# Optimization experiments

Measured on AMD Instinct MI355X. Metric: run time of the kernel, lower is better.

Reference implementation:

```python
import jax, jax.numpy as jnp
import numpy as np
import math

N, E, D, H = 1536, 49152, 512, 8
DH = D // H  # head dim = 64
SCALE = 256.0 * math.sqrt(2.0)  # rel_dists scaling in forward


def sinusoidal_pe(x, d):
    """x: [...] float positions -> [..., d] interleaved sin/cos encoding."""
    div = jnp.exp(jnp.arange(0, d, 2, dtype=jnp.float32) * (-math.log(10000.0) / d))
    ang = x[..., None] * div  # [..., d//2]
    return jnp.stack([jnp.sin(ang), jnp.cos(ang)], axis=-1).reshape(*x.shape, d)


def setup_inputs() -> dict:
    key = jax.random.key(0)
    ks = jax.random.split(key, 8)
    features = jax.random.normal(ks[0], (N, D), dtype=jnp.float32)
    edge_index = jax.random.randint(ks[1], (2, E), 0, N, dtype=jnp.int64)
    edge_attr = jax.random.uniform(ks[2], (E,), dtype=jnp.float32)  # normalized distances
    pos = jax.random.uniform(ks[3], (N, 2), dtype=jnp.float32)  # unused by forward
    s = 1.0 / math.sqrt(D)  # ~xavier-uniform bound sqrt(6/(D+D))... use simple symmetric init
    Wq = jax.random.uniform(ks[4], (D, D), minval=-s, maxval=s, dtype=jnp.float32)
    Wk = jax.random.uniform(ks[5], (D, D), minval=-s, maxval=s, dtype=jnp.float32)
    Wv = jax.random.uniform(ks[6], (D, D), minval=-s, maxval=s, dtype=jnp.float32)
    bq = jnp.zeros((D,), jnp.float32)
    bk = jnp.zeros((D,), jnp.float32)
    bv = jnp.zeros((D,), jnp.float32)
    return dict(features=features, edge_index=edge_index, edge_attr=edge_attr, pos=pos,
                Wq=Wq, bq=bq, Wk=Wk, bk=bk, Wv=Wv, bv=bv)


def reference(features, edge_index, edge_attr, pos, Wq, bq, Wk, bk, Wv, bv):
    # batch dim is 1 in the original (features.unsqueeze(0)); we omit it.
    q = (features @ Wq.T + bq).reshape(N, H, DH).transpose(1, 0, 2)  # [H,N,DH]
    k = (features @ Wk.T + bk).reshape(N, H, DH).transpose(1, 0, 2)
    v = (features @ Wv.T + bv).reshape(N, H, DH).transpose(1, 0, 2)

    qk = jnp.einsum('hqd,hrd->hqr', q, k)  # [H,N,N]

    # to_dense_adj: scatter-add edge_attr into dense [N,N], then scale
    rel = jnp.zeros((N, N), jnp.float32).at[edge_index[0], edge_index[1]].add(edge_attr) * SCALE
    # embed_k and embed_q are identical parameter-free sinusoidal encodings of rel
    rk = sinusoidal_pe(rel, DH)  # [N,N,DH]

    # original: qk + q.rk + k.rq + (q_repeat*k_repeat == qk)  => 2*qk + q.rk + k.rk
    logits = 2.0 * qk \
        + jnp.einsum('hqd,qrd->hqr', q, rk) \
        + jnp.einsum('hrd,qrd->hqr', k, rk)
    attn = jax.nn.softmax(logits / math.sqrt(DH), axis=-1)  # [H,N,N]

    out = jnp.einsum('hqr,hrd->hqd', attn, v)  # [H,N,DH]
    out = out.transpose(1, 0, 2).reshape(N, D)  # [N,D]
    return out.max(axis=0)  # [D] max-pool over nodes (MIL pooling)
```

## Files before the change

kernel.cpp:

```cpp
#include <hip/hip_runtime.h>
#include <cmath>


constexpr int Nn  = 1536;
constexpr int Dd  = 512;
constexpr int Hh  = 8;
constexpr int DHd = 64;
constexpr int SPLITS = 8;
constexpr float SCALE_F = 362.03867196751236f;
constexpr float M0 = 8.0f;
constexpr unsigned short NOEDGE = 0xFFFFu;

typedef float f4 __attribute__((ext_vector_type(4)));
typedef int   i4 __attribute__((ext_vector_type(4)));
typedef int   i2 __attribute__((ext_vector_type(2)));
typedef __attribute__((ext_vector_type(4))) float f32x4;
typedef __attribute__((ext_vector_type(8))) short bf16x8;

__device__ inline unsigned short bf16_rne(float x) {
    unsigned u = __float_as_uint(x);
    unsigned r = u + 0x7fff + ((u >> 16) & 1);
    return (unsigned short)(r >> 16);
}
__device__ inline float bf16_tof(unsigned short h) {
    return __uint_as_float(((unsigned)h) << 16);
}

__global__ __launch_bounds__(256) void pack_fw_k(
    const float* __restrict__ feat,
    const float* __restrict__ Wq, const float* __restrict__ Wk, const float* __restrict__ Wv,
    unsigned short* __restrict__ pFh, unsigned short* __restrict__ pFl,
    unsigned short* __restrict__ pWh, unsigned short* __restrict__ pWl)
{
    int tg = blockIdx.x * 256 + threadIdx.x;
    int type = blockIdx.y;
    int L = tg & 63;
    int kc = (tg >> 6) & 15;
    int t10 = tg >> 10;
    const float* src;
    unsigned short *oh, *ol;
    int row, col;
    if (type == 0) {
        src = feat; oh = pFh; ol = pFl;
        row = t10 * 16 + (L & 15);
        col = kc * 32 + (L >> 4) * 8;
    } else {
        int z = t10 >> 5, nt = t10 & 31;
        src = (z == 0) ? Wq : (z == 1) ? Wk : Wv;
        oh = pWh; ol = pWl;
        row = nt * 16 + (L & 15);
        col = kc * 32 + (L >> 4) * 8;
    }
    f4 a = *(const f4*)(src + (size_t)row * Dd + col);
    f4 b = *(const f4*)(src + (size_t)row * Dd + col + 4);
    float x[8];
    #pragma unroll
    for (int j = 0; j < 4; ++j) { x[j] = a[j]; x[4 + j] = b[j]; }
    unsigned short hs[8], ls[8];
    #pragma unroll
    for (int j = 0; j < 8; ++j) {
        hs[j] = bf16_rne(x[j]);
        ls[j] = bf16_rne(x[j] - bf16_tof(hs[j]));
    }
    *(bf16x8*)(oh + (size_t)tg * 8) = *(bf16x8*)hs;
    *(bf16x8*)(ol + (size_t)tg * 8) = *(bf16x8*)ls;
}

__global__ __launch_bounds__(256) void qkvm_k(
    const unsigned short* __restrict__ pFh, const unsigned short* __restrict__ pFl,
    const unsigned short* __restrict__ pWh, const unsigned short* __restrict__ pWl,
    const float* __restrict__ bq, const float* __restrict__ bk, const float* __restrict__ bv,
    float* __restrict__ Qo, float* __restrict__ Ko, float* __restrict__ Vo)
{
    const int lin = blockIdx.x + 8 * (blockIdx.y + 24 * blockIdx.z);
    const int swz = (lin & 7) * 72 + (lin >> 3);
    const int bx  = swz & 7;
    const int rem = swz >> 3;
    const int by  = rem % 24;
    const int bz  = rem / 24;

    const float* __restrict__ bias = (bz == 0) ? bq : (bz == 1) ? bk : bv;
    float* __restrict__ outp       = (bz == 0) ? Qo : (bz == 1) ? Ko : Vo;
    const int tid = threadIdx.x;
    const int L = tid & 63, wv = tid >> 6;
    const int l15 = L & 15, quad = L >> 4;
    const int mt0 = by * 4 + (wv & 1) * 2;
    const int nt0 = bx * 4 + (wv >> 1) * 2;

    f32x4 acc[2][2];
    #pragma unroll
    for (int i = 0; i < 2; ++i)
        #pragma unroll
        for (int j = 0; j < 2; ++j) acc[i][j] = (f32x4){0.f, 0.f, 0.f, 0.f};

    for (int kc = 0; kc < 16; ++kc) {
        bf16x8 ah[2], al[2], bh[2], bl[2];
        #pragma unroll
        for (int i = 0; i < 2; ++i) {
            size_t ao = ((size_t)((mt0 + i) * 16 + kc)) * 512 + L * 8;
            ah[i] = *(const bf16x8*)(pFh + ao);
            al[i] = *(const bf16x8*)(pFl + ao);
            size_t bo = ((size_t)((bz * 32 + nt0 + i) * 16 + kc)) * 512 + L * 8;
            bh[i] = *(const bf16x8*)(pWh + bo);
            bl[i] = *(const bf16x8*)(pWl + bo);
        }
        #pragma unroll
        for (int i = 0; i < 2; ++i)
            #pragma unroll
            for (int j = 0; j < 2; ++j) {
                f32x4 a = acc[i][j];
                a = __builtin_amdgcn_mfma_f32_16x16x32_bf16(ah[i], bh[j], a, 0, 0, 0);
                a = __builtin_amdgcn_mfma_f32_16x16x32_bf16(ah[i], bl[j], a, 0, 0, 0);
                a = __builtin_amdgcn_mfma_f32_16x16x32_bf16(al[i], bh[j], a, 0, 0, 0);
                a = __builtin_amdgcn_mfma_f32_16x16x32_bf16(al[i], bl[j], a, 0, 0, 0);
                acc[i][j] = a;
            }
    }

    #pragma unroll
    for (int i = 0; i < 2; ++i) {
        int row0 = (mt0 + i) * 16 + quad * 4;
        #pragma unroll
        for (int j = 0; j < 2; ++j) {
            int col = (nt0 + j) * 16 + l15;
            float b = bias[col];
            #pragma unroll
            for (int reg = 0; reg < 4; ++reg)
                outp[(size_t)(row0 + reg) * Dd + col] = acc[i][j][reg] + b;
        }
    }
}

__global__ __launch_bounds__(256) void pack_k(
    const float* __restrict__ Q, const float* __restrict__ K, const float* __restrict__ V,
    unsigned short* __restrict__ pQh, unsigned short* __restrict__ pQl,
    unsigned short* __restrict__ pKh, unsigned short* __restrict__ pKl,
    unsigned short* __restrict__ pVh, unsigned short* __restrict__ pVl)
{
    int tg = blockIdx.x * 256 + threadIdx.x;
    int type = blockIdx.y;
    int L = tg & 63;
    float x[8];
    unsigned short* oh;
    unsigned short* ol;
    if (type < 2) {
        const float* src = type ? K : Q;
        oh = type ? pKh : pQh;
        ol = type ? pKl : pQl;
        int kc = (tg >> 6) & 1;
        int mt = (tg >> 7) % 96;
        int h  = (tg >> 7) / 96;
        int row = mt * 16 + (L & 15);
        int col = h * 64 + kc * 32 + (L >> 4) * 8;
        f4 a = *(const f4*)(src + (size_t)row * Dd + col);
        f4 b = *(const f4*)(src + (size_t)row * Dd + col + 4);
        float sc = type ? 1.0f : 0.25f;
        #pragma unroll
        for (int j = 0; j < 4; ++j) { x[j] = a[j] * sc; x[4 + j] = b[j] * sc; }
    } else {
        oh = pVh; ol = pVl;
        int dt = (tg >> 6) & 3;
        int rc = (tg >> 8) % 48;
        int h  = (tg >> 8) / 48;
        int col  = h * 64 + dt * 16 + (L & 15);
        int row0 = rc * 32 + (L >> 4) * 8;
        #pragma unroll
        for (int j = 0; j < 8; ++j) x[j] = V[(size_t)(row0 + j) * Dd + col];
    }
    unsigned short hs[8], ls[8];
    #pragma unroll
    for (int j = 0; j < 8; ++j) {
        hs[j] = bf16_rne(x[j]);
        ls[j] = bf16_rne(x[j] - bf16_tof(hs[j]));
    }
    *(bf16x8*)(oh + (size_t)tg * 8) = *(bf16x8*)hs;
    *(bf16x8*)(ol + (size_t)tg * 8) = *(bf16x8*)ls;
}

__global__ __launch_bounds__(256) void init_rel_k(float* __restrict__ rel,
                                                  unsigned short* __restrict__ eid)
{
    size_t i = ((size_t)blockIdx.x * 256 + threadIdx.x) * 4;
    if (i < (size_t)Nn * Nn) {
        *(f4*)(rel + i) = (f4){0.f, 0.f, 0.f, 0.f};
        *(i2*)(eid + i) = (i2){-1, -1};
    }
}

__global__ __launch_bounds__(256) void scatter_k(
    const int* __restrict__ raw, const float* __restrict__ attr,
    float* __restrict__ rel, unsigned short* __restrict__ eid,
    int* __restrict__ idxn, int E)
{
    int e = blockIdx.x * 256 + threadIdx.x;
    if (e >= E) return;
    int acc = 0;
    #pragma unroll
    for (int i = 0; i < 16; ++i) acc |= raw[2 * i + 1];
    int s, t;
    if (acc == 0) { s = raw[2 * e]; t = raw[2 * (E + e)]; }
    else          { s = raw[e];     t = raw[E + e]; }
    idxn[e] = s; idxn[E + e] = t;
    size_t off = (size_t)s * Nn + t;
    atomicAdd(rel + off, attr[e] * SCALE_F);
    eid[off] = (unsigned short)e;
}

__global__ void oddsum_k(const float* __restrict__ Q, const float* __restrict__ K,
                         float* __restrict__ qodd, float* __restrict__ kodd,
                         float* __restrict__ koddT)
{
    int t = blockIdx.x * 256 + threadIdx.x;
    if (t >= 2 * Nn * Hh) return;
    const float* src = (t < Nn * Hh) ? Q : K;
    int i = (t < Nn * Hh) ? t : t - Nn * Hh;
    int n = i >> 3, h = i & 7;
    const float* row = src + (size_t)n * Dd + h * DHd;
    float s = 0.f;
    #pragma unroll
    for (int ii = 0; ii < 32; ++ii) s += row[2 * ii + 1];
    if (t < Nn * Hh) qodd[i] = s;
    else { kodd[i] = s; koddT[h * Nn + n] = 0.125f * s; }
}

__global__ __launch_bounds__(256) void delta2_k(
    const int* __restrict__ idxn, const float* __restrict__ rel,
    const float* __restrict__ Q, const float* __restrict__ K,
    const float* __restrict__ qodd, const float* __restrict__ kodd,
    float* __restrict__ delta8, int E)
{
    const int w = threadIdx.x >> 6;
    const int e = blockIdx.x * 4 + w;
    if (e >= E) return;
    const int j = threadIdx.x & 63;
    const int qi = idxn[e], ri = idxn[E + e];
    const float x = rel[(size_t)qi * Nn + ri];
    const float dj = __expf(-0.28782313662425572f * (float)(j >> 1));
    float sj, cj;
    __sincosf(x * dj, &sj, &cj);
    const float tj = (j & 1) ? cj : sj;
    const float* qrow = Q + (size_t)qi * Dd;
    const float* krow = K + (size_t)ri * Dd;
    float out = 0.f;
    #pragma unroll
    for (int h = 0; h < 8; ++h) {
        float v = (qrow[h * 64 + j] + krow[h * 64 + j]) * tj;
        #pragma unroll
        for (int o = 1; o < 64; o <<= 1) v += __shfl_xor(v, o);
        if (j == h) out = v;
    }
    if (j < 8)
        delta8[(size_t)e * Hh + j] = 0.125f * (out - qodd[qi * Hh + j] - kodd[ri * Hh + j]);
}

__global__ __launch_bounds__(256, 2) void flash6_k(
    const unsigned short* __restrict__ pQh, const unsigned short* __restrict__ pQl,
    const unsigned short* __restrict__ pKh, const unsigned short* __restrict__ pKl,
    const unsigned short* __restrict__ pVh, const unsigned short* __restrict__ pVl,
    const unsigned short* __restrict__ eid, const float* __restrict__ delta8,
    const float* __restrict__ koddT,
    float* __restrict__ Opart, float* __restrict__ Lpart)
{
    const int lin = blockIdx.x + 24 * (blockIdx.y + 8 * blockIdx.z);
    const int swz = (lin & 7) * 192 + (lin >> 3);
    const int qtb = swz % 24;
    const int hs  = swz / 24;
    const int h   = hs & 7;
    const int s   = hs >> 3;

    const int w   = threadIdx.x >> 6;
    const int qt  = qtb * 4 + w;
    const int L   = threadIdx.x & 63, quad = L >> 4, l15 = L & 15;
    const int q0  = qt * 16;
    __shared__ unsigned short phi[4][16][80];
    __shared__ unsigned short plo[4][16][80];

    bf16x8 qh[2], ql[2];
    #pragma unroll
    for (int kc = 0; kc < 2; ++kc) {
        size_t off = ((size_t)((h * 96 + qt) * 2 + kc)) * 512 + L * 8;
        qh[kc] = *(const bf16x8*)(pQh + off);
        ql[kc] = *(const bf16x8*)(pQl + off);
    }

    f32x4 O[4];
    float lsum[4];
    #pragma unroll
    for (int r = 0; r < 4; ++r) { lsum[r] = 0.f; O[r] = (f32x4){0.f, 0.f, 0.f, 0.f}; }

    const int NT = 24 / SPLITS;
    const int Tbase = s * NT;

    bf16x8 kh0[4], kh1[4], kl0[4], kl1[4];
    {
        const int r0 = Tbase * 64;
        #pragma unroll
        for (int nt = 0; nt < 4; ++nt) {
            size_t b0 = ((size_t)((h * 96 + (r0 >> 4) + nt) * 2)) * 512 + L * 8;
            kh0[nt] = *(const bf16x8*)(pKh + b0);
            kh1[nt] = *(const bf16x8*)(pKh + b0 + 512);
            kl0[nt] = *(const bf16x8*)(pKl + b0);
            kl1[nt] = *(const bf16x8*)(pKl + b0 + 512);
        }
    }

    float kvcur[4], dcur[16];
    {
        const int r0 = Tbase * 64;
        unsigned ecur[16];
        #pragma unroll
        for (int nt = 0; nt < 4; ++nt) {
            kvcur[nt] = koddT[h * Nn + r0 + nt * 16 + l15];
            #pragma unroll
            for (int reg = 0; reg < 4; ++reg)
                ecur[nt * 4 + reg] = eid[(size_t)(q0 + quad * 4 + reg) * Nn + r0 + nt * 16 + l15];
        }
        #pragma unroll
        for (int i = 0; i < 16; ++i) {
            unsigned e = ecur[i];
            float d = 0.f;
            if (e != NOEDGE) d = delta8[(size_t)e * Hh + h];
            dcur[i] = d;
        }
    }

    for (int T = 0; T < NT; ++T) {
        const int r0 = (Tbase + T) * 64;
        const bool more = (T + 1 < NT);

        unsigned enxt[16];
        float kvnxt[4];
        if (more) {
            const int r1 = r0 + 64;
            #pragma unroll
            for (int nt = 0; nt < 4; ++nt) {
                kvnxt[nt] = koddT[h * Nn + r1 + nt * 16 + l15];
                #pragma unroll
                for (int reg = 0; reg < 4; ++reg)
                    enxt[nt * 4 + reg] = eid[(size_t)(q0 + quad * 4 + reg) * Nn + r1 + nt * 16 + l15];
            }
        }

        bf16x8 vh0[4], vh1[4], vl0[4], vl1[4];
        #pragma unroll
        for (int dt = 0; dt < 4; ++dt) {
            size_t vb = ((size_t)((h * 48 + (r0 >> 5)) * 4 + dt)) * 512 + L * 8;
            vh0[dt] = *(const bf16x8*)(pVh + vb);
            vh1[dt] = *(const bf16x8*)(pVh + vb + 2048);
            vl0[dt] = *(const bf16x8*)(pVl + vb);
            vl1[dt] = *(const bf16x8*)(pVl + vb + 2048);
        }

        f32x4 S[4];
        #pragma unroll
        for (int nt = 0; nt < 4; ++nt) {
            f32x4 a = {0.f, 0.f, 0.f, 0.f};
            a = __builtin_amdgcn_mfma_f32_16x16x32_bf16(qh[0], kh0[nt], a, 0, 0, 0);
            a = __builtin_amdgcn_mfma_f32_16x16x32_bf16(qh[1], kh1[nt], a, 0, 0, 0);
            a = __builtin_amdgcn_mfma_f32_16x16x32_bf16(qh[0], kl0[nt], a, 0, 0, 0);
            a = __builtin_amdgcn_mfma_f32_16x16x32_bf16(qh[1], kl1[nt], a, 0, 0, 0);
            a = __builtin_amdgcn_mfma_f32_16x16x32_bf16(ql[0], kh0[nt], a, 0, 0, 0);
            a = __builtin_amdgcn_mfma_f32_16x16x32_bf16(ql[1], kh1[nt], a, 0, 0, 0);
            S[nt] = a;
        }

        if (more) {
            const int r1 = r0 + 64;
            #pragma unroll
            for (int nt = 0; nt < 4; ++nt) {
                size_t b0 = ((size_t)((h * 96 + (r1 >> 4) + nt) * 2)) * 512 + L * 8;
                kh0[nt] = *(const bf16x8*)(pKh + b0);
                kh1[nt] = *(const bf16x8*)(pKh + b0 + 512);
                kl0[nt] = *(const bf16x8*)(pKl + b0);
                kl1[nt] = *(const bf16x8*)(pKl + b0 + 512);
            }
        }

        #pragma unroll
        for (int reg = 0; reg < 4; ++reg) {
            float p[4];
            #pragma unroll
            for (int nt = 0; nt < 4; ++nt) {
                p[nt] = __expf(S[nt][reg] + kvcur[nt] + dcur[nt * 4 + reg] - M0);
                lsum[reg] += p[nt];
                unsigned short hi = bf16_rne(p[nt]);
                phi[w][quad * 4 + reg][nt * 16 + l15] = hi;
                plo[w][quad * 4 + reg][nt * 16 + l15] = bf16_rne(p[nt] - bf16_tof(hi));
            }
        }

        bf16x8 ph[2], pl[2];
        #pragma unroll
        for (int kc2 = 0; kc2 < 2; ++kc2) {
            ph[kc2] = *(const bf16x8*)&phi[w][l15][kc2 * 32 + quad * 8];
            pl[kc2] = *(const bf16x8*)&plo[w][l15][kc2 * 32 + quad * 8];
        }

        #pragma unroll
        for (int dt = 0; dt < 4; ++dt) {
            f32x4 a = O[dt];
            a = __builtin_amdgcn_mfma_f32_16x16x32_bf16(ph[0], vh0[dt], a, 0, 0, 0);
            a = __builtin_amdgcn_mfma_f32_16x16x32_bf16(ph[1], vh1[dt], a, 0, 0, 0);
            a = __builtin_amdgcn_mfma_f32_16x16x32_bf16(ph[0], vl0[dt], a, 0, 0, 0);
            a = __builtin_amdgcn_mfma_f32_16x16x32_bf16(ph[1], vl1[dt], a, 0, 0, 0);
            a = __builtin_amdgcn_mfma_f32_16x16x32_bf16(pl[0], vh0[dt], a, 0, 0, 0);
            a = __builtin_amdgcn_mfma_f32_16x16x32_bf16(pl[1], vh1[dt], a, 0, 0, 0);
            O[dt] = a;
        }

        if (more) {
            #pragma unroll
            for (int i = 0; i < 16; ++i) {
                unsigned e = enxt[i];
                float d = 0.f;
                if (e != NOEDGE) d = delta8[(size_t)e * Hh + h];
                dcur[i] = d;
            }
            #pragma unroll
            for (int nt = 0; nt < 4; ++nt) kvcur[nt] = kvnxt[nt];
        }
    }

    #pragma unroll
    for (int reg = 0; reg < 4; ++reg) {
        #pragma unroll
        for (int o = 1; o < 16; o <<= 1) lsum[reg] += __shfl_xor(lsum[reg], o);
    }

    #pragma unroll
    for (int dt = 0; dt < 4; ++dt)
        #pragma unroll
        for (int reg = 0; reg < 4; ++reg)
            Opart[((size_t)(s * Hh + h) * Nn + q0 + quad * 4 + reg) * 64 + dt * 16 + l15] = O[dt][reg];
    if (l15 == 0) {
        #pragma unroll
        for (int reg = 0; reg < 4; ++reg)
            Lpart[(size_t)(s * Hh + h) * Nn + q0 + quad * 4 + reg] = lsum[reg];
    }
}

__global__ __launch_bounds__(256) void combine_mp_k(
    const float* __restrict__ Opart, const float* __restrict__ Lpart,
    float* __restrict__ partial)
{
    const int b = blockIdx.x;
    const int t = threadIdx.x;
    const int cg = (t & 127) * 4;
    const int h = cg >> 6, d = cg & 63;
    const int rh = t >> 7;
    f4 mx = {-3.0e38f, -3.0e38f, -3.0e38f, -3.0e38f};
    for (int r = 0; r < 2; ++r) {
        int q = b * 4 + rh * 2 + r;
        float l = 0.f;
        f4 o = {0.f, 0.f, 0.f, 0.f};
        #pragma unroll
        for (int s2 = 0; s2 < SPLITS; ++s2) {
            l += Lpart[(size_t)(s2 * Hh + h) * Nn + q];
            f4 ov = *(const f4*)(Opart + ((size_t)(s2 * Hh + h) * Nn + q) * 64 + d);
            #pragma unroll
            for (int c = 0; c < 4; ++c) o[c] += ov[c];
        }
        float inv = 1.0f / l;
        #pragma unroll
        for (int c = 0; c < 4; ++c) mx[c] = fmaxf(mx[c], o[c] * inv);
    }
    *(f4*)(partial + (size_t)(b * 2 + rh) * 512 + cg) = mx;
}

__global__ __launch_bounds__(128) void mp2a_k(const float* __restrict__ partial,
                                              float* __restrict__ partial2)
{
    const int b = blockIdx.x;
    const int t = threadIdx.x;
    f4 mx = {-3.0e38f, -3.0e38f, -3.0e38f, -3.0e38f};
    for (int i = 0; i < 24; ++i) {
        f4 v = *(const f4*)(partial + (size_t)(b * 24 + i) * 512 + 4 * t);
        #pragma unroll
        for (int c = 0; c < 4; ++c) mx[c] = fmaxf(mx[c], v[c]);
    }
    *(f4*)(partial2 + (size_t)b * 512 + 4 * t) = mx;
}

__global__ __launch_bounds__(128) void mp2b_k(const float* __restrict__ partial2,
                                              float* __restrict__ outp)
{
    const int t = threadIdx.x;
    f4 mx = {-3.0e38f, -3.0e38f, -3.0e38f, -3.0e38f};
    for (int b = 0; b < 32; ++b) {
        f4 v = *(const f4*)(partial2 + (size_t)b * 512 + 4 * t);
        #pragma unroll
        for (int c = 0; c < 4; ++c) mx[c] = fmaxf(mx[c], v[c]);
    }
    *(f4*)(outp + 4 * t) = mx;
}

extern "C" void kernel_launch(void* const* d_in, const int* in_sizes, int n_in,
                              void* d_out, int out_size, void* d_ws, size_t ws_size,
                              hipStream_t stream)
{
    const float* feat   = (const float*)d_in[0];
    const int*   rawidx = (const int*)d_in[1];
    const float* attr   = (const float*)d_in[2];
    const float* Wq = (const float*)d_in[4];
    const float* bq = (const float*)d_in[5];
    const float* Wk = (const float*)d_in[6];
    const float* bk = (const float*)d_in[7];
    const float* Wv = (const float*)d_in[8];
    const float* bv = (const float*)d_in[9];
    float* outp = (float*)d_out;
    const int E = in_sizes[2];

    const size_t ND_ = (size_t)Nn * Dd;
    const size_t NN_ = (size_t)Nn * Nn;
    const size_t PK_ = (size_t)Hh * 96 * 2 * 512;

    float* ws    = (float*)d_ws;
    float* Q     = ws;
    float* K     = Q + ND_;
    float* V     = K + ND_;
    float* rel   = V + ND_;
    unsigned short* pFh = (unsigned short*)(rel + NN_);
    unsigned short* pFl = pFh + PK_;
    unsigned short* pWh = pFl + PK_;
    unsigned short* pWl = pWh + PK_;
    unsigned short* eid = (unsigned short*)(pWl + PK_);
    float* delta8 = (float*)(eid + NN_);
    float* qodd  = delta8 + (size_t)E * Hh;
    float* kodd  = qodd + (size_t)Nn * Hh;
    float* koddT = kodd + (size_t)Nn * Hh;
    int*   idxn  = (int*)(koddT + (size_t)Nn * Hh);
    unsigned short* pQh = (unsigned short*)(idxn + 2 * E);
    unsigned short* pQl = pQh + PK_;
    unsigned short* pKh = pQl + PK_;
    unsigned short* pKl = pKh + PK_;
    unsigned short* pVh = pKl + PK_;
    unsigned short* pVl = pVh + PK_;
    float* Lpart = (float*)(pVl + PK_);
    float* partial = Lpart + (size_t)SPLITS * Hh * Nn;
    float* partial2 = partial + (size_t)768 * 512;
    float* Opart = ws;

    pack_fw_k<<<dim3(384, 2), 256, 0, stream>>>(feat, Wq, Wk, Wv, pFh, pFl, pWh, pWl);
    qkvm_k<<<dim3(8, 24, 3), 256, 0, stream>>>(pFh, pFl, pWh, pWl, bq, bk, bv, Q, K, V);
    init_rel_k<<<(int)((NN_ / 4 + 255) / 256), 256, 0, stream>>>(rel, eid);
    scatter_k<<<(E + 255) / 256, 256, 0, stream>>>(rawidx, attr, rel, eid, idxn, E);
    oddsum_k<<<(2 * Nn * Hh + 255) / 256, 256, 0, stream>>>(Q, K, qodd, kodd, koddT);
    delta2_k<<<(E + 3) / 4, 256, 0, stream>>>(idxn, rel, Q, K, qodd, kodd, delta8, E);
    pack_k<<<dim3(384, 3), 256, 0, stream>>>(Q, K, V, pQh, pQl, pKh, pKl, pVh, pVl);
    flash6_k<<<dim3(24, 8, SPLITS), 256, 0, stream>>>(pQh, pQl, pKh, pKl, pVh, pVl,
                                                      eid, delta8, koddT, Opart, Lpart);
    combine_mp_k<<<384, 256, 0, stream>>>(Opart, Lpart, partial);
    mp2a_k<<<32, 128, 0, stream>>>(partial, partial2);
    mp2b_k<<<1, 128, 0, stream>>>(partial2, outp);
}
```

Before: 185.1 us.

## Process two query tiles per wave to reuse K/V fragments in flash kernel

Each wave now handles two 16-row query tiles instead of one, so every K and V fragment loaded from global memory feeds twice as many MFMAs. The grid shrinks from 24 to 12 blocks along x to keep total coverage. This halves K/V global traffic per query, but roughly doubles register pressure (two sets of Q, S, O, delta arrays) and halves block count to 768, which may reduce occupancy or latency hiding.

Result: slower. 344.7 us (+86.2%).

```diff
diff --git a/kernel.cpp b/kernel.cpp
--- a/kernel.cpp
+++ b/kernel.cpp
@@ -253,7 +253,7 @@
         delta8[(size_t)e * Hh + j] = 0.125f * (out - qodd[qi * Hh + j] - kodd[ri * Hh + j]);
 }
 
-__global__ __launch_bounds__(256, 2) void flash6_k(
+__global__ __launch_bounds__(256, 2) void flash7_k(
     const unsigned short* __restrict__ pQh, const unsigned short* __restrict__ pQl,
     const unsigned short* __restrict__ pKh, const unsigned short* __restrict__ pKl,
     const unsigned short* __restrict__ pVh, const unsigned short* __restrict__ pVl,
@@ -261,32 +261,39 @@
     const float* __restrict__ koddT,
     float* __restrict__ Opart, float* __restrict__ Lpart)
 {
-    const int lin = blockIdx.x + 24 * (blockIdx.y + 8 * blockIdx.z);
-    const int swz = (lin & 7) * 192 + (lin >> 3);
-    const int qtb = swz % 24;
-    const int hs  = swz / 24;
+    const int lin = blockIdx.x + 12 * (blockIdx.y + 8 * blockIdx.z);
+    const int swz = (lin & 7) * 96 + (lin >> 3);
+    const int qtb = swz % 12;
+    const int hs  = swz / 12;
     const int h   = hs & 7;
     const int s   = hs >> 3;
 
     const int w   = threadIdx.x >> 6;
-    const int qt  = qtb * 4 + w;
+    const int qtA = (qtb * 4 + w) * 2;
     const int L   = threadIdx.x & 63, quad = L >> 4, l15 = L & 15;
-    const int q0  = qt * 16;
-    __shared__ unsigned short phi[4][16][80];
-    __shared__ unsigned short plo[4][16][80];
-
-    bf16x8 qh[2], ql[2];
+    const int q0A = qtA * 16;
+    __shared__ unsigned short phi[4][2][16][80];
+    __shared__ unsigned short plo[4][2][16][80];
+
+    bf16x8 qhA[2], qlA[2], qhB[2], qlB[2];
     #pragma unroll
     for (int kc = 0; kc < 2; ++kc) {
-        size_t off = ((size_t)((h * 96 + qt) * 2 + kc)) * 512 + L * 8;
-        qh[kc] = *(const bf16x8*)(pQh + off);
-        ql[kc] = *(const bf16x8*)(pQl + off);
-    }
-
-    f32x4 O[4];
-    float lsum[4];
-    #pragma unroll
-    for (int r = 0; r < 4; ++r) { lsum[r] = 0.f; O[r] = (f32x4){0.f, 0.f, 0.f, 0.f}; }
+        size_t offA = ((size_t)((h * 96 + qtA) * 2 + kc)) * 512 + L * 8;
+        qhA[kc] = *(const bf16x8*)(pQh + offA);
+        qlA[kc] = *(const bf16x8*)(pQl + offA);
+        size_t offB = ((size_t)((h * 96 + qtA + 1) * 2 + kc)) * 512 + L * 8;
+        qhB[kc] = *(const bf16x8*)(pQh + offB);
+        qlB[kc] = *(const bf16x8*)(pQl + offB);
+    }
+
+    f32x4 OA[4], OB[4];
+    float lsA[4], lsB[4];
+    #pragma unroll
+    for (int r = 0; r < 4; ++r) {
+        lsA[r] = 0.f; lsB[r] = 0.f;
+        OA[r] = (f32x4){0.f, 0.f, 0.f, 0.f};
+        OB[r] = (f32x4){0.f, 0.f, 0.f, 0.f};
+    }
 
     const int NT = 24 / SPLITS;
     const int Tbase = s * NT;
@@ -304,23 +311,33 @@
         }
     }
 
-    float kvcur[4], dcur[16];
+    float kvcur[4], dcurA[16], dcurB[16];
     {
         const int r0 = Tbase * 64;
-        unsigned ecur[16];
+        unsigned ecA[16], ecB[16];
         #pragma unroll
         for (int nt = 0; nt < 4; ++nt) {
             kvcur[nt] = koddT[h * Nn + r0 + nt * 16 + l15];
             #pragma unroll
-            for (int reg = 0; reg < 4; ++reg)
-                ecur[nt * 4 + reg] = eid[(size_t)(q0 + quad * 4 + reg) * Nn + r0 + nt * 16 + l15];
+            for (int reg = 0; reg < 4; ++reg) {
+                size_t rr = (size_t)(r0 + nt * 16 + l15);
+                ecA[nt * 4 + reg] = eid[(size_t)(q0A + quad * 4 + reg) * Nn + rr];
+                ecB[nt * 4 + reg] = eid[(size_t)(q0A + 16 + quad * 4 + reg) * Nn + rr];
+            }
         }
         #pragma unroll
         for (int i = 0; i < 16; ++i) {
-            unsigned e = ecur[i];
+            unsigned e = ecA[i];
             float d = 0.f;
             if (e != NOEDGE) d = delta8[(size_t)e * Hh + h];
-            dcur[i] = d;
+            dcurA[i] = d;
+        }
+        #pragma unroll
+        for (int i = 0; i < 16; ++i) {
+            unsigned e = ecB[i];
+            float d = 0.f;
+            if (e != NOEDGE) d = delta8[(size_t)e * Hh + h];
+            dcurB[i] = d;
         }
     }
 
@@ -328,7 +345,7 @@
         const int r0 = (Tbase + T) * 64;
         const bool more = (T + 1 < NT);
 
-        unsigned enxt[16];
+        unsigned enA[16], enB[16];
         float kvnxt[4];
         if (more) {
             const int r1 = r0 + 64;
@@ -336,8 +353,11 @@
             for (int nt = 0; nt < 4; ++nt) {
                 kvnxt[nt] = koddT[h * Nn + r1 + nt * 16 + l15];
                 #pragma unroll
-                for (int reg = 0; reg < 4; ++reg)
-                    enxt[nt * 4 + reg] = eid[(size_t)(q0 + quad * 4 + reg) * Nn + r1 + nt * 16 + l15];
+                for (int reg = 0; reg < 4; ++reg) {
+                    size_t rr = (size_t)(r1 + nt * 16 + l15);
+                    enA[nt * 4 + reg] = eid[(size_t)(q0A + quad * 4 + reg) * Nn + rr];
+                    enB[nt * 4 + reg] = eid[(size_t)(q0A + 16 + quad * 4 + reg) * Nn + rr];
+                }
             }
         }
 
@@ -351,17 +371,25 @@
             vl1[dt] = *(const bf16x8*)(pVl + vb + 2048);
         }
 
-        f32x4 S[4];
+        f32x4 SA[4], SB[4];
         #pragma unroll
         for (int nt = 0; nt < 4; ++nt) {
             f32x4 a = {0.f, 0.f, 0.f, 0.f};
-            a = __builtin_amdgcn_mfma_f32_16x16x32_bf16(qh[0], kh0[nt], a, 0, 0, 0);
-            a = __builtin_amdgcn_mfma_f32_16x16x32_bf16(qh[1], kh1[nt], a, 0, 0, 0);
-            a = __builtin_amdgcn_mfma_f32_16x16x32_bf16(qh[0], kl0[nt], a, 0, 0, 0);
-            a = __builtin_amdgcn_mfma_f32_16x16x32_bf16(qh[1], kl1[nt], a, 0, 0, 0);
-            a = __builtin_amdgcn_mfma_f32_16x16x32_bf16(ql[0], kh0[nt], a, 0, 0, 0);
-            a = __builtin_amdgcn_mfma_f32_16x16x32_bf16(ql[1], kh1[nt], a, 0, 0, 0);
-            S[nt] = a;
+            a = __builtin_amdgcn_mfma_f32_16x16x32_bf16(qhA[0], kh0[nt], a, 0, 0, 0);
+            a = __builtin_amdgcn_mfma_f32_16x16x32_bf16(qhA[1], kh1[nt], a, 0, 0, 0);
+            a = __builtin_amdgcn_mfma_f32_16x16x32_bf16(qhA[0], kl0[nt], a, 0, 0, 0);
+            a = __builtin_amdgcn_mfma_f32_16x16x32_bf16(qhA[1], kl1[nt], a, 0, 0, 0);
+            a = __builtin_amdgcn_mfma_f32_16x16x32_bf16(qlA[0], kh0[nt], a, 0, 0, 0);
+            a = __builtin_amdgcn_mfma_f32_16x16x32_bf16(qlA[1], kh1[nt], a, 0, 0, 0);
+            SA[nt] = a;
+            f32x4 b = {0.f, 0.f, 0.f, 0.f};
+            b = __builtin_amdgcn_mfma_f32_16x16x32_bf16(qhB[0], kh0[nt], b, 0, 0, 0);
+            b = __builtin_amdgcn_mfma_f32_16x16x32_bf16(qhB[1], kh1[nt], b, 0, 0, 0);
+            b = __builtin_amdgcn_mfma_f32_16x16x32_bf16(qhB[0], kl0[nt], b, 0, 0, 0);
+            b = __builtin_amdgcn_mfma_f32_16x16x32_bf16(qhB[1], kl1[nt], b, 0, 0, 0);
+            b = __builtin_amdgcn_mfma_f32_16x16x32_bf16(qlB[0], kh0[nt], b, 0, 0, 0);
+            b = __builtin_amdgcn_mfma_f32_16x16x32_bf16(qlB[1], kh1[nt], b, 0, 0, 0);
+            SB[nt] = b;
         }
 
         if (more) {
@@ -381,40 +409,79 @@
             float p[4];
             #pragma unroll
             for (int nt = 0; nt < 4; ++nt) {
-                p[nt] = __expf(S[nt][reg] + kvcur[nt] + dcur[nt * 4 + reg] - M0);
-                lsum[reg] += p[nt];
+                p[nt] = __expf(SA[nt][reg] + kvcur[nt] + dcurA[nt * 4 + reg] - M0);
+                lsA[reg] += p[nt];
                 unsigned short hi = bf16_rne(p[nt]);
-                phi[w][quad * 4 + reg][nt * 16 + l15] = hi;
-                plo[w][quad * 4 + reg][nt * 16 + l15] = bf16_rne(p[nt] - bf16_tof(hi));
-            }
-        }
-
-        bf16x8 ph[2], pl[2];
-        #pragma unroll
-        for (int kc2 = 0; kc2 < 2; ++kc2) {
-            ph[kc2] = *(const bf16x8*)&phi[w][l15][kc2 * 32 + quad * 8];
-            pl[kc2] = *(const bf16x8*)&plo[w][l15][kc2 * 32 + quad * 8];
-        }
-
-        #pragma unroll
-        for (int dt = 0; dt < 4; ++dt) {
-            f32x4 a = O[dt];
-            a = __builtin_amdgcn_mfma_f32_16x16x32_bf16(ph[0], vh0[dt], a, 0, 0, 0);
-            a = __builtin_amdgcn_mfma_f32_16x16x32_bf16(ph[1], vh1[dt], a, 0, 0, 0);
-            a = __builtin_amdgcn_mfma_f32_16x16x32_bf16(ph[0], vl0[dt], a, 0, 0, 0);
-            a = __builtin_amdgcn_mfma_f32_16x16x32_bf16(ph[1], vl1[dt], a, 0, 0, 0);
-            a = __builtin_amdgcn_mfma_f32_16x16x32_bf16(pl[0], vh0[dt], a, 0, 0, 0);
-            a = __builtin_amdgcn_mfma_f32_16x16x32_bf16(pl[1], vh1[dt], a, 0, 0, 0);
-            O[dt] = a;
+                phi[w][0][quad * 4 + reg][nt * 16 + l15] = hi;
+                plo[w][0][quad * 4 + reg][nt * 16 + l15] = bf16_rne(p[nt] - bf16_tof(hi));
+            }
+        }
+        {
+            bf16x8 ph[2], pl[2];
+            #pragma unroll
+            for (int kc2 = 0; kc2 < 2; ++kc2) {
+                ph[kc2] = *(const bf16x8*)&phi[w][0][l15][kc2 * 32 + quad * 8];
+                pl[kc2] = *(const bf16x8*)&plo[w][0][l15][kc2 * 32 + quad * 8];
+            }
+            #pragma unroll
+            for (int dt = 0; dt < 4; ++dt) {
+                f32x4 a = OA[dt];
+                a = __builtin_amdgcn_mfma_f32_16x16x32_bf16(ph[0], vh0[dt], a, 0, 0, 0);
+                a = __builtin_amdgcn_mfma_f32_16x16x32_bf16(ph[1], vh1[dt], a, 0, 0, 0);
+                a = __builtin_amdgcn_mfma_f32_16x16x32_bf16(ph[0], vl0[dt], a, 0, 0, 0);
+                a = __builtin_amdgcn_mfma_f32_16x16x32_bf16(ph[1], vl1[dt], a, 0, 0, 0);
+                a = __builtin_amdgcn_mfma_f32_16x16x32_bf16(pl[0], vh0[dt], a, 0, 0, 0);
+                a = __builtin_amdgcn_mfma_f32_16x16x32_bf16(pl[1], vh1[dt], a, 0, 0, 0);
+                OA[dt] = a;
+            }
+        }
+
+        #pragma unroll
+        for (int reg = 0; reg < 4; ++reg) {
+            float p[4];
+            #pragma unroll
+            for (int nt = 0; nt < 4; ++nt) {
+                p[nt] = __expf(SB[nt][reg] + kvcur[nt] + dcurB[nt * 4 + reg] - M0);
+                lsB[reg] += p[nt];
+                unsigned short hi = bf16_rne(p[nt]);
+                phi[w][1][quad * 4 + reg][nt * 16 + l15] = hi;
+                plo[w][1][quad * 4 + reg][nt * 16 + l15] = bf16_rne(p[nt] - bf16_tof(hi));
+            }
+        }
+        {
+            bf16x8 ph[2], pl[2];
+            #pragma unroll
+            for (int kc2 = 0; kc2 < 2; ++kc2) {
+                ph[kc2] = *(const bf16x8*)&phi[w][1][l15][kc2 * 32 + quad * 8];
+                pl[kc2] = *(const bf16x8*)&plo[w][1][l15][kc2 * 32 + quad * 8];
+            }
+            #pragma unroll
+            for (int dt = 0; dt < 4; ++dt) {
+                f32x4 b = OB[dt];
+                b = __builtin_amdgcn_mfma_f32_16x16x32_bf16(ph[0], vh0[dt], b, 0, 0, 0);
+                b = __builtin_amdgcn_mfma_f32_16x16x32_bf16(ph[1], vh1[dt], b, 0, 0, 0);
+                b = __builtin_amdgcn_mfma_f32_16x16x32_bf16(ph[0], vl0[dt], b, 0, 0, 0);
+                b = __builtin_amdgcn_mfma_f32_16x16x32_bf16(ph[1], vl1[dt], b, 0, 0, 0);
+                b = __builtin_amdgcn_mfma_f32_16x16x32_bf16(pl[0], vh0[dt], b, 0, 0, 0);
+                b = __builtin_amdgcn_mfma_f32_16x16x32_bf16(pl[1], vh1[dt], b, 0, 0, 0);
+                OB[dt] = b;
+            }
         }
 
         if (more) {
             #pragma unroll
             for (int i = 0; i < 16; ++i) {
-                unsigned e = enxt[i];
+                unsigned e = enA[i];
                 float d = 0.f;
                 if (e != NOEDGE) d = delta8[(size_t)e * Hh + h];
-                dcur[i] = d;
+                dcurA[i] = d;
+            }
+            #pragma unroll
+            for (int i = 0; i < 16; ++i) {
+                unsigned e = enB[i];
+                float d = 0.f;
+                if (e != NOEDGE) d = delta8[(size_t)e * Hh + h];
+                dcurB[i] = d;
             }
             #pragma unroll
             for (int nt = 0; nt < 4; ++nt) kvcur[nt] = kvnxt[nt];
@@ -424,18 +491,25 @@
     #pragma unroll
     for (int reg = 0; reg < 4; ++reg) {
         #pragma unroll
-        for (int o = 1; o < 16; o <<= 1) lsum[reg] += __shfl_xor(lsum[reg], o);
+        for (int o = 1; o < 16; o <<= 1) {
+            lsA[reg] += __shfl_xor(lsA[reg], o);
+            lsB[reg] += __shfl_xor(lsB[reg], o);
+        }
     }
 
     #pragma unroll
     for (int dt = 0; dt < 4; ++dt)
         #pragma unroll
-        for (int reg = 0; reg < 4; ++reg)
-            Opart[((size_t)(s * Hh + h) * Nn + q0 + quad * 4 + reg) * 64 + dt * 16 + l15] = O[dt][reg];
+        for (int reg = 0; reg < 4; ++reg) {
+            Opart[((size_t)(s * Hh + h) * Nn + q0A + quad * 4 + reg) * 64 + dt * 16 + l15] = OA[dt][reg];
+            Opart[((size_t)(s * Hh + h) * Nn + q0A + 16 + quad * 4 + reg) * 64 + dt * 16 + l15] = OB[dt][reg];
+        }
     if (l15 == 0) {
         #pragma unroll
-        for (int reg = 0; reg < 4; ++reg)
-            Lpart[(size_t)(s * Hh + h) * Nn + q0 + quad * 4 + reg] = lsum[reg];
+        for (int reg = 0; reg < 4; ++reg) {
+            Lpart[(size_t)(s * Hh + h) * Nn + q0A + quad * 4 + reg] = lsA[reg];
+            Lpart[(size_t)(s * Hh + h) * Nn + q0A + 16 + quad * 4 + reg] = lsB[reg];
+        }
     }
 }
 
@@ -547,7 +621,7 @@
     oddsum_k<<<(2 * Nn * Hh + 255) / 256, 256, 0, stream>>>(Q, K, qodd, kodd, koddT);
     delta2_k<<<(E + 3) / 4, 256, 0, stream>>>(idxn, rel, Q, K, qodd, kodd, delta8, E);
     pack_k<<<dim3(384, 3), 256, 0, stream>>>(Q, K, V, pQh, pQl, pKh, pKl, pVh, pVl);
-    flash6_k<<<dim3(24, 8, SPLITS), 256, 0, stream>>>(pQh, pQl, pKh, pKl, pVh, pVl,
+    flash7_k<<<dim3(12, 8, SPLITS), 256, 0, stream>>>(pQh, pQl, pKh, pKl, pVh, pVl,
                                                       eid, delta8, koddT, Opart, Lpart);
     combine_mp_k<<<384, 256, 0, stream>>>(Opart, Lpart, partial);
     mp2a_k<<<32, 128, 0, stream>>>(partial, partial2);
```
